# Optimization experiments

Hardware: AMD Instinct MI355X
Metric: run time of the kernel (lower is better)

## Reference

```python
import jax, jax.numpy as jnp
from jax import lax
import numpy as np

DN = ('NCH', 'OIH', 'NCH')  # conv dimension numbers


def _dw_conv(x, w, stride, pad):
    # depthwise conv1d: x (B,Cin,T), w (Cout, k), groups = Cin
    C = x.shape[1]
    return lax.conv_general_dilated(x, w[:, None, :], (stride,), [(pad, pad)],
                                    feature_group_count=C, dimension_numbers=DN)


def _polyphase_upsample(x, up_w, ratio=2):
    # faithful to _polyphase_upsample_fused: pad (2,3), grouped conv (C -> C*ratio, k=6),
    # interleave the `ratio` phases along time, crop 2 from each side
    B, C, T = x.shape
    xp = jnp.pad(x, ((0, 0), (0, 0), (2, 3)))
    out = _dw_conv(xp, up_w, 1, 0)                     # (B, C*ratio, T)
    out = out.reshape(B, C, ratio, T).transpose(0, 1, 3, 2).reshape(B, C, ratio * T)
    return out[..., 2:-2]


def _snake_beta(x, alpha, beta):
    # SnakeBeta with alpha_logscale=True: x + (1 - cos(2*e^a*x)) / (2*e^b + 1e-9)
    a = jnp.exp(alpha)[None, :, None]
    inv_2b = 1.0 / (2.0 * jnp.exp(beta)[None, :, None] + 1e-9)
    return x + (1.0 - jnp.cos(2.0 * a * x)) * inv_2b


def _activation1d(x, up_w, down_w, alpha, beta):
    x = _polyphase_upsample(x, up_w, 2)                # (B, C, 2T-4)
    x = _snake_beta(x, alpha, beta)
    return _dw_conv(x, down_w, 2, 5)                   # stride-2 lowpass -> (B, C, T-2)


def _conv1d(x, w, b, dilation, pad):
    y = lax.conv_general_dilated(x, w, (1,), [(pad, pad)], rhs_dilation=(dilation,),
                                 dimension_numbers=DN)
    return y + b[None, :, None]


def setup_inputs() -> dict:
    key = jax.random.key(0)
    ks = jax.random.split(key, 13)
    B, C, T = 8, 512, 8192
    f32 = jnp.float32
    return {
        'x': jax.random.normal(ks[0], (B, C, T), f32),
        'up_w1': jax.random.normal(ks[1], (2 * C, 6), f32) * 0.2,
        'down_w1': jax.random.normal(ks[2], (C, 12), f32) * 0.2,
        'alpha1': jax.random.normal(ks[3], (C,), f32) * 0.1,
        'beta1': jax.random.normal(ks[4], (C,), f32) * 0.1,
        'up_w2': jax.random.normal(ks[5], (2 * C, 6), f32) * 0.2,
        'down_w2': jax.random.normal(ks[6], (C, 12), f32) * 0.2,
        'alpha2': jax.random.normal(ks[7], (C,), f32) * 0.1,
        'beta2': jax.random.normal(ks[8], (C,), f32) * 0.1,
        'c1_w': jax.random.normal(ks[9], (C, C, 3), f32) * 0.01,
        'c1_b': jnp.zeros((C,), f32),
        'c2_w': jax.random.normal(ks[10], (C, C, 3), f32) * 0.01,
        'c2_b': jnp.zeros((C,), f32),
    }


def reference(x, up_w1, down_w1, alpha1, beta1, up_w2, down_w2, alpha2, beta2,
              c1_w, c1_b, c2_w, c2_b):
    # AMPBlock0 forward: a1 -> c1 (dilation=dilation[0]=1, pad=1) -> a2 -> c2 (pad=1) -> residual
    xt = _activation1d(x, up_w1, down_w1, alpha1, beta1)   # (B,C,T-2)
    xt = _conv1d(xt, c1_w, c1_b, 1, 1)                     # (B,C,T-2)
    xt = _activation1d(xt, up_w2, down_w2, alpha2, beta2)  # (B,C,T-4)
    xt = _conv1d(xt, c2_w, c2_b, 1, 1)                     # (B,C,T-4)
    return xt + x[:, :, :xt.shape[2]]
```

## Files before the change

kernel.cpp:

```cpp
#include <hip/hip_runtime.h>
#include <math.h>

#define CC 512
#define BB 8
#define TTOT 8192
#define LEN1 (TTOT - 2)
#define LEN2 (TTOT - 4)
#define GPRE 8
#define GPOST 24
#define PITCH (GPRE + TTOT + GPOST)
#define CHST (PITCH * 32)
#define BST (PITCH * 512)

typedef unsigned short u16;
typedef __bf16 v8bf __attribute__((ext_vector_type(8)));
typedef float v4f __attribute__((ext_vector_type(4)));

__device__ __forceinline__ u16 f2b(float f) {
    unsigned u = __float_as_uint(f);
    unsigned r = (u + 0x7FFFu + ((u >> 16) & 1u)) >> 16;
    return (u16)r;
}
__device__ __forceinline__ float b2f(u16 h) {
    return __uint_as_float(((unsigned)h) << 16);
}
__device__ __forceinline__ void ldsdma16(const void* g, void* l) {
    __builtin_amdgcn_global_load_lds(
        (const __attribute__((address_space(1))) unsigned int*)g,
        (__attribute__((address_space(3))) unsigned int*)l, 16, 0, 0);
}


__global__ __launch_bounds__(256) void wprep_kernel(const float* __restrict__ w,
                                                    u16* __restrict__ wr)
{
    int idx = blockIdx.x * 256 + threadIdx.x;
    int co = idx >> 9, ci = idx & 511;
    const float* s = w + (size_t)idx * 3;
    int g = (ci >> 3) & 3;
    int slot = ((g ^ ((co >> 1) & 3)) << 3) | (ci & 7);
    size_t base = (size_t)(ci >> 5) * 3 * 16384 + (size_t)co * 32 + slot;
#pragma unroll
    for (int k = 0; k < 3; ++k)
        wr[base + (size_t)k * 16384] = f2b(s[k]);
}

__global__ __launch_bounds__(256) void zguard_kernel(u16* x0, int Lstart)
{
    int r = blockIdx.x;
    int b = blockIdx.y;
    int R = (r < GPRE) ? r : (GPRE + Lstart + (r - GPRE));
    unsigned* p = (unsigned*)(x0 + (size_t)b * BST);
    int chunk = threadIdx.x >> 4, off = threadIdx.x & 15;
    p[(size_t)chunk * (CHST / 2) + (size_t)R * 16 + off] = 0u;
}

template<bool TMAJ>
__global__ __launch_bounds__(256) void actS_kernel(
    const void* __restrict__ xin_v,
    u16* __restrict__ yout,
    const float* __restrict__ up_w,
    const float* __restrict__ down_w,
    const float* __restrict__ alpha,
    const float* __restrict__ beta,
    int Lin)
{
    const int Lout = Lin - 2;
    const int smax = 2 * Lin - 4;
    const int tid  = threadIdx.x;
    const int cs   = tid & 31;
    const int tseg = tid >> 5;
    const int chunk = blockIdx.y;
    const int b     = blockIdx.z;
    const int T0    = blockIdx.x * 128;
    const int Tt    = T0 + tseg * 16;
    const int cg    = chunk * 32 + cs;

    __shared__ float xs[32 * 141];

    if (!TMAJ) {
        const float* xcb = (const float*)xin_v + ((size_t)b * CC + chunk * 32) * (size_t)Lin;
        int lane = tid & 63, w = tid >> 6;
#pragma unroll
        for (int rr = 0; rr < 8; ++rr) {
            int c = w * 8 + rr;
            const float* xr = xcb + (size_t)c * Lin;
            for (int i = lane; i < 139; i += 64) {
                int g = T0 - 4 + i;
                xs[c * 141 + i] = (g >= 0 && g < Lin) ? xr[g] : 0.0f;
            }
        }
    } else {
        const u16* xb = (const u16*)xin_v + (size_t)b * BST + (size_t)chunk * CHST;
        int pr = tid & 15, rq = tid >> 4;
#pragma unroll
        for (int r0 = 0; r0 < 139; r0 += 16) {
            int row = r0 + rq;
            if (row < 139) {
                int R = GPRE + T0 - 4 + row;
                unsigned u = *((const unsigned*)(xb + (size_t)R * 32) + pr);
                int p2 = pr * 2;
                int c = (((p2 >> 3) ^ ((R >> 1) & 3)) << 3) | (p2 & 7);
                xs[c * 141 + row]       = b2f((u16)(u & 0xFFFFu));
                xs[(c + 1) * 141 + row] = b2f((u16)(u >> 16));
            }
        }
    }
    __syncthreads();

    const float a     = expf(alpha[cg]);
    const float inv2b = 1.0f / (2.0f * expf(beta[cg]) + 1e-9f);
    float uwa[6], uwb[6], dw[12];
#pragma unroll
    for (int k = 0; k < 6; ++k) {
        uwa[k] = up_w[(2 * cg) * 6 + k];
        uwb[k] = up_w[(2 * cg + 1) * 6 + k];
    }
#pragma unroll
    for (int j = 0; j < 12; ++j) dw[j] = down_w[cg * 12 + j];

    const float* xrow = xs + cs * 141 + tseg * 16;

    float xw[12], sr[12];

    auto sval = [&](int idx) -> float {
        int s  = 2 * Tt - 5 + idx;
        int xo = (idx + 1) >> 1;
        float u = 0.0f;
#pragma unroll
        for (int k = 0; k < 6; ++k) {
            float wk = (idx & 1) ? uwa[k] : uwb[k];
            u = fmaf(xw[(xo + k) % 12], wk, u);
        }
        float v = fmaf(1.0f - __cosf(2.0f * a * u), inv2b, u);
        return (s >= 0 && s < smax) ? v : 0.0f;
    };

#pragma unroll
    for (int j = 0; j < 11; ++j) xw[j] = xrow[j];
    xw[11] = 0.0f;
#pragma unroll
    for (int idx = 0; idx < 10; ++idx) sr[idx] = sval(idx);

    u16* yb = yout + (size_t)b * BST + (size_t)chunk * CHST;

#pragma unroll
    for (int i = 0; i < 16; ++i) {
        xw[(11 + i) % 12] = xrow[11 + i];
        sr[(10 + 2 * i) % 12] = sval(10 + 2 * i);
        sr[(11 + 2 * i) % 12] = sval(11 + 2 * i);
        float y = 0.0f;
#pragma unroll
        for (int j = 0; j < 12; ++j)
            y = fmaf(sr[(2 * i + j) % 12], dw[j], y);
        int t = Tt + i;
        if (t < Lout) {
            int R = GPRE + t;
            int slot = (((cs >> 3) ^ ((R >> 1) & 3)) << 3) | (cs & 7);
            yb[(size_t)R * 32 + slot] = f2b(y);
        }
    }
}

template<int ORIENT>
__global__ __launch_bounds__(256, 2) void convg_kernel(
    const u16* __restrict__ xt,
    const u16* __restrict__ wr,
    const float* __restrict__ bias,
    u16* __restrict__ yt,
    float* __restrict__ out,
    const float* __restrict__ resid,
    int Lout)
{
    const int tid  = threadIdx.x;
    const int lane = tid & 63, wid = tid >> 6;
    const int wt = wid & 1, wc = wid >> 1;
    const int l15 = lane & 15, q = lane >> 4;
    const int t0  = blockIdx.x * 256;
    const int co0 = blockIdx.y * 128;
    const int b   = blockIdx.z;

    __shared__ __align__(16) u16 xsm[264 * 32];
    __shared__ __align__(16) u16 wsm[3 * 128 * 32];

    const u16* xb = xt + (size_t)b * BST;
    const int R0 = GPRE + t0 - 1;

    v4f acc[8][4];
#pragma unroll
    for (int m = 0; m < 8; ++m)
#pragma unroll
        for (int n = 0; n < 4; ++n)
#pragma unroll
            for (int r = 0; r < 4; ++r) acc[m][n][r] = 0.0f;

    for (int cig = 0; cig < 16; ++cig) {
        const u16* xsl = xb + (size_t)cig * CHST + (size_t)R0 * 32;
        const u16* wsl = wr + (size_t)cig * 49152 + (size_t)co0 * 32;

#pragma unroll
        for (int j = 0; j < 5; ++j) {
            int ii = wid + 4 * j;
            if (ii < 17) {
                if (ii * 64 + lane < 1056)
                    ldsdma16(xsl + (size_t)(ii * 64 + lane) * 8, xsm + (size_t)ii * 512);
            }
        }
#pragma unroll
        for (int j = 0; j < 6; ++j) {
            int ii = wid + 4 * j;
            ldsdma16(wsl + (size_t)(ii * 64 + lane) * 8 + (size_t)(ii >> 3) * 12288,
                     wsm + (size_t)ii * 512);
        }
        __syncthreads();

#pragma unroll
        for (int k = 0; k < 3; ++k) {
            v8bf wf[4];
#pragma unroll
            for (int n = 0; n < 4; ++n) {
                int co_l = wc * 64 + n * 16 + l15;
                wf[n] = *(const v8bf*)(wsm + ((k * 128 + co_l) << 5)
                                           + ((q ^ ((co_l >> 1) & 3)) << 3));
            }
#pragma unroll
            for (int m = 0; m < 8; ++m) {
                int r = wt * 128 + m * 16 + l15 + k;
                v8bf xf = *(const v8bf*)(xsm + (r << 5)
                                             + ((q ^ (((r + 7) >> 1) & 3)) << 3));
#pragma unroll
                for (int n = 0; n < 4; ++n) {
                    if (ORIENT == 0)
                        acc[m][n] = __builtin_amdgcn_mfma_f32_16x16x32_bf16(
                            xf, wf[n], acc[m][n], 0, 0, 0);
                    else
                        acc[m][n] = __builtin_amdgcn_mfma_f32_16x16x32_bf16(
                            wf[n], xf, acc[m][n], 0, 0, 0);
                }
            }
        }
        __syncthreads();
    }

    if (ORIENT == 0) {
        float bv[4];
#pragma unroll
        for (int n = 0; n < 4; ++n) bv[n] = bias[co0 + wc * 64 + n * 16 + l15];
        u16* yb = yt + (size_t)b * BST;
        int cb = (co0 + wc * 64) >> 5;
#pragma unroll
        for (int m = 0; m < 8; ++m) {
            int tb = t0 + wt * 128 + m * 16;
#pragma unroll
            for (int rg = 0; rg < 4; ++rg) {
                int t = tb + q * 4 + rg;
                if (t < Lout) {
                    int R = GPRE + t;
                    int f = (R >> 1) & 3;
#pragma unroll
                    for (int n = 0; n < 4; ++n) {
                        int cl = ((n & 1) << 4) | l15;
                        int slot = (((cl >> 3) ^ f) << 3) | (cl & 7);
                        yb[(size_t)(cb + (n >> 1)) * CHST + (size_t)R * 32 + slot]
                            = f2b(acc[m][n][rg] + bv[n]);
                    }
                }
            }
        }
    } else {
        float bv[4][4];
#pragma unroll
        for (int n = 0; n < 4; ++n)
#pragma unroll
            for (int rg = 0; rg < 4; ++rg)
                bv[n][rg] = bias[co0 + wc * 64 + n * 16 + q * 4 + rg];
#pragma unroll
        for (int n = 0; n < 4; ++n) {
#pragma unroll
            for (int rg = 0; rg < 4; ++rg) {
                int co = co0 + wc * 64 + n * 16 + q * 4 + rg;
                float* orow = out + ((size_t)b * CC + co) * Lout;
                const float* rrow = resid + ((size_t)b * CC + co) * TTOT;
#pragma unroll
                for (int m = 0; m < 8; ++m) {
                    int t = t0 + wt * 128 + m * 16 + l15;
                    if (t < Lout)
                        orow[t] = acc[m][n][rg] + bv[n][rg] + rrow[t];
                }
            }
        }
    }
}

extern "C" void kernel_launch(void* const* d_in, const int* in_sizes, int n_in,
                              void* d_out, int out_size, void* d_ws, size_t ws_size,
                              hipStream_t stream)
{
    const float* x       = (const float*)d_in[0];
    const float* up_w1   = (const float*)d_in[1];
    const float* down_w1 = (const float*)d_in[2];
    const float* alpha1  = (const float*)d_in[3];
    const float* beta1   = (const float*)d_in[4];
    const float* up_w2   = (const float*)d_in[5];
    const float* down_w2 = (const float*)d_in[6];
    const float* alpha2  = (const float*)d_in[7];
    const float* beta2   = (const float*)d_in[8];
    const float* c1_w    = (const float*)d_in[9];
    const float* c1_b    = (const float*)d_in[10];
    const float* c2_w    = (const float*)d_in[11];
    const float* c2_b    = (const float*)d_in[12];
    float* out = (float*)d_out;

    u16* wr1 = (u16*)d_ws;
    u16* wr2 = wr1 + 786432;
    u16* xTa = wr2 + 786432;
    u16* xTb = xTa + (size_t)BB * BST;

    wprep_kernel<<<1024, 256, 0, stream>>>(c1_w, wr1);
    wprep_kernel<<<1024, 256, 0, stream>>>(c2_w, wr2);
    zguard_kernel<<<dim3(32, 8), 256, 0, stream>>>(xTa, LEN1);
    zguard_kernel<<<dim3(32, 8), 256, 0, stream>>>(xTb, LEN1);

    actS_kernel<false><<<dim3(64, 16, 8), 256, 0, stream>>>(
        (const void*)x, xTa, up_w1, down_w1, alpha1, beta1, TTOT);
    convg_kernel<0><<<dim3(32, 4, 8), 256, 0, stream>>>(
        xTa, wr1, c1_b, xTb, nullptr, nullptr, LEN1);
    zguard_kernel<<<dim3(32, 8), 256, 0, stream>>>(xTa, LEN2);
    actS_kernel<true><<<dim3(64, 16, 8), 256, 0, stream>>>(
        (const void*)xTb, xTa, up_w2, down_w2, alpha2, beta2, LEN1);
    convg_kernel<1><<<dim3(32, 4, 8), 256, 0, stream>>>(
        xTa, wr2, c2_b, nullptr, out, x, LEN2);
}
```

Baseline: 647.6 us.

## Double-buffer conv LDS staging and widen block to 256 output channels

The grouped-conv MFMA kernel now uses 512 threads covering 256 output channels per block, so each staged input tile is reused across twice as many channels. LDS tiles are double-buffered, with the next channel group prefetched via LDS DMA while the current one is computed, and synchronized with an explicit vmcnt wait and s_barrier. A dummy padding load evens out the per-wave outstanding load count, and MFMA issue is wrapped in raised priority with fragments preloaded. Shared memory use rises substantially, which may limit how many blocks fit per CU.

```diff
diff --git a/kernel.cpp b/kernel.cpp
--- a/kernel.cpp
+++ b/kernel.cpp
@@ -163,7 +163,7 @@
 }
 
 template<int ORIENT>
-__global__ __launch_bounds__(256, 2) void convg_kernel(
+__global__ __launch_bounds__(512, 2) void convg_kernel(
     const u16* __restrict__ xt,
     const u16* __restrict__ wr,
     const float* __restrict__ bias,
@@ -177,11 +177,12 @@
     const int wt = wid & 1, wc = wid >> 1;
     const int l15 = lane & 15, q = lane >> 4;
     const int t0  = blockIdx.x * 256;
-    const int co0 = blockIdx.y * 128;
+    const int co0 = blockIdx.y * 256;
     const int b   = blockIdx.z;
 
-    __shared__ __align__(16) u16 xsm[264 * 32];
-    __shared__ __align__(16) u16 wsm[3 * 128 * 32];
+    __shared__ __align__(16) u16 xsm[2][264 * 32];
+    __shared__ __align__(16) u16 wsm[2][3 * 256 * 32];
+    __shared__ __align__(16) u16 dpad[512];
 
     const u16* xb = xt + (size_t)b * BST;
     const int R0 = GPRE + t0 - 1;
@@ -194,52 +195,77 @@
 #pragma unroll
             for (int r = 0; r < 4; ++r) acc[m][n][r] = 0.0f;
 
-    for (int cig = 0; cig < 16; ++cig) {
+    auto stage = [&](int cig, int sel) {
         const u16* xsl = xb + (size_t)cig * CHST + (size_t)R0 * 32;
         const u16* wsl = wr + (size_t)cig * 49152 + (size_t)co0 * 32;
-
-#pragma unroll
-        for (int j = 0; j < 5; ++j) {
-            int ii = wid + 4 * j;
+        u16* xd = &xsm[sel][0];
+        u16* wd = &wsm[sel][0];
+#pragma unroll
+        for (int j = 0; j < 3; ++j) {
+            int ii = wid + 8 * j;
             if (ii < 17) {
                 if (ii * 64 + lane < 1056)
-                    ldsdma16(xsl + (size_t)(ii * 64 + lane) * 8, xsm + (size_t)ii * 512);
-            }
-        }
+                    ldsdma16(xsl + (size_t)(ii * 64 + lane) * 8, xd + (size_t)ii * 512);
+            }
+        }
+        if (wid != 0) ldsdma16(xsl + (size_t)lane * 8, &dpad[0]);
 #pragma unroll
         for (int j = 0; j < 6; ++j) {
-            int ii = wid + 4 * j;
-            ldsdma16(wsl + (size_t)(ii * 64 + lane) * 8 + (size_t)(ii >> 3) * 12288,
-                     wsm + (size_t)ii * 512);
-        }
-        __syncthreads();
-
+            int ii = wid + 8 * j;
+            ldsdma16(wsl + (size_t)(ii >> 4) * 16384
+                         + (size_t)((ii & 15) * 64 + lane) * 8,
+                     wd + (size_t)ii * 512);
+        }
+    };
+
+    stage(0, 0);
+    int cur = 0;
+#pragma unroll 1
+    for (int cig = 0; cig < 16; ++cig) {
+        if (cig < 15) {
+            stage(cig + 1, cur ^ 1);
+            __builtin_amdgcn_sched_barrier(0);
+            asm volatile("s_waitcnt vmcnt(9)" ::: "memory");
+        } else {
+            asm volatile("s_waitcnt vmcnt(0)" ::: "memory");
+        }
+        __builtin_amdgcn_s_barrier();
+        __builtin_amdgcn_sched_barrier(0);
+
+        const u16* xs = &xsm[cur][0];
+        const u16* ws = &wsm[cur][0];
 #pragma unroll
         for (int k = 0; k < 3; ++k) {
-            v8bf wf[4];
+            v8bf wf[4], xfr[8];
 #pragma unroll
             for (int n = 0; n < 4; ++n) {
                 int co_l = wc * 64 + n * 16 + l15;
-                wf[n] = *(const v8bf*)(wsm + ((k * 128 + co_l) << 5)
-                                           + ((q ^ ((co_l >> 1) & 3)) << 3));
+                wf[n] = *(const v8bf*)(ws + ((k * 256 + co_l) << 5)
+                                          + ((q ^ ((co_l >> 1) & 3)) << 3));
             }
 #pragma unroll
             for (int m = 0; m < 8; ++m) {
                 int r = wt * 128 + m * 16 + l15 + k;
-                v8bf xf = *(const v8bf*)(xsm + (r << 5)
-                                             + ((q ^ (((r + 7) >> 1) & 3)) << 3));
+                xfr[m] = *(const v8bf*)(xs + (r << 5)
+                                           + ((q ^ (((r + 7) >> 1) & 3)) << 3));
+            }
+            __builtin_amdgcn_s_setprio(1);
+#pragma unroll
+            for (int m = 0; m < 8; ++m)
 #pragma unroll
                 for (int n = 0; n < 4; ++n) {
                     if (ORIENT == 0)
                         acc[m][n] = __builtin_amdgcn_mfma_f32_16x16x32_bf16(
-                            xf, wf[n], acc[m][n], 0, 0, 0);
+                            xfr[m], wf[n], acc[m][n], 0, 0, 0);
                     else
                         acc[m][n] = __builtin_amdgcn_mfma_f32_16x16x32_bf16(
-                            wf[n], xf, acc[m][n], 0, 0, 0);
+                            wf[n], xfr[m], acc[m][n], 0, 0, 0);
                 }
-            }
-        }
-        __syncthreads();
+            __builtin_amdgcn_s_setprio(0);
+        }
+        __builtin_amdgcn_sched_barrier(0);
+        __builtin_amdgcn_s_barrier();
+        cur ^= 1;
     }
 
     if (ORIENT == 0) {
@@ -323,11 +349,11 @@
 
     actS_kernel<false><<<dim3(64, 16, 8), 256, 0, stream>>>(
         (const void*)x, xTa, up_w1, down_w1, alpha1, beta1, TTOT);
-    convg_kernel<0><<<dim3(32, 4, 8), 256, 0, stream>>>(
+    convg_kernel<0><<<dim3(32, 2, 8), 512, 0, stream>>>(
         xTa, wr1, c1_b, xTb, nullptr, nullptr, LEN1);
     zguard_kernel<<<dim3(32, 8), 256, 0, stream>>>(xTa, LEN2);
     actS_kernel<true><<<dim3(64, 16, 8), 256, 0, stream>>>(
         (const void*)xTb, xTa, up_w2, down_w2, alpha2, beta2, LEN1);
-    convg_kernel<1><<<dim3(32, 4, 8), 256, 0, stream>>>(
+    convg_kernel<1><<<dim3(32, 2, 8), 512, 0, stream>>>(
         xTa, wr2, c2_b, nullptr, out, x, LEN2);
 }
```

Result: no change. 657.1 us (+1.5%).
